# Kernel tuning notes

Measured on AMD Instinct MI355X. Metric: run time of the kernel, lower is better.

## Reference

```python
import jax, jax.numpy as jnp
import numpy as np

L, C = 32768, 512
EPS = 1e-5

def _layernorm(x, w, b):
    mu = jnp.mean(x, axis=-1, keepdims=True)
    var = jnp.mean(jnp.square(x - mu), axis=-1, keepdims=True)
    return (x - mu) * jax.lax.rsqrt(var + EPS) * w + b

def _scan(u, decay):
    # inclusive first-order linear scan: b_t = decay * b_{t-1} + u_t
    a = jnp.broadcast_to(decay, u.shape)
    def combine(l, r):
        return (l[0] * r[0], r[1] + r[0] * l[1])
    _, b = jax.lax.associative_scan(combine, (a, u), axis=0)
    return b

def setup_inputs() -> dict:
    key = jax.random.key(0)
    ks = jax.random.split(key, 8)
    s = 0.02
    return {
        "x": jax.random.normal(ks[0], (L, C), dtype=jnp.float32),
        "ln1_w": jnp.ones((C,), jnp.float32),
        "ln1_b": jnp.zeros((C,), jnp.float32),
        "W_in": jax.random.normal(ks[1], (C, C), jnp.float32) * s,
        "b_in": jnp.zeros((C,), jnp.float32),
        "W_gate": jax.random.normal(ks[2], (C, C), jnp.float32) * s,
        "b_gate": jnp.zeros((C,), jnp.float32),
        "W_out": jax.random.normal(ks[3], (C, C), jnp.float32) * s,
        "b_out": jnp.zeros((C,), jnp.float32),
        "decay_logit": jnp.zeros((C,), jnp.float32),  # torch init: zeros -> sigmoid = 0.5
        "ln2_w": jnp.ones((C,), jnp.float32),
        "ln2_b": jnp.zeros((C,), jnp.float32),
        "W_ff1": jax.random.normal(ks[4], (C, 2 * C), jnp.float32) * s,
        "b_ff1": jnp.zeros((2 * C,), jnp.float32),
        "W_ff2": jax.random.normal(ks[5], (2 * C, C), jnp.float32) * s,
        "b_ff2": jnp.zeros((C,), jnp.float32),
    }

def reference(x, ln1_w, ln1_b, W_in, b_in, W_gate, b_gate, W_out, b_out,
              decay_logit, ln2_w, ln2_b, W_ff1, b_ff1, W_ff2, b_ff2):
    hidden = _layernorm(x, ln1_w, ln1_b)
    u = hidden @ W_in + b_in
    gate = jax.nn.sigmoid(hidden @ W_gate + b_gate)
    decay = jax.nn.sigmoid(decay_logit)
    fwd = _scan(u, decay) * gate
    bwd = jnp.flip(_scan(jnp.flip(u, axis=0), decay), axis=0) * gate
    state_out = 0.5 * (fwd + bwd)
    x = x + state_out @ W_out + b_out
    h = _layernorm(x, ln2_w, ln2_b)
    x = x + jax.nn.silu(h @ W_ff1 + b_ff1) @ W_ff2 + b_ff2
    return x
```

## Files before the change

kernel.cpp:

```cpp
#include <hip/hip_runtime.h>
#include <stdint.h>


#define L_SEQ 32768
#define CDIM 512
#define LN_EPS 1e-5f
#define CHUNK 64
#define NCHUNK (L_SEQ / CHUNK)

typedef __attribute__((ext_vector_type(8))) short short8;
typedef __attribute__((ext_vector_type(4))) float floatx4;

__device__ inline unsigned short f2bf(float f) {
  union { float f; unsigned int u; } v; v.f = f;
  unsigned int r = v.u + 0x7fffu + ((v.u >> 16) & 1u);
  return (unsigned short)(r >> 16);
}
__device__ inline float bf2f(unsigned short h) {
  union { float f; unsigned int u; } v; v.u = ((unsigned int)h) << 16;
  return v.f;
}
__device__ inline float sigmoidf_(float x) { return 1.0f / (1.0f + __expf(-x)); }

__device__ __forceinline__ void gll16(const void* g, void* l) {
  __builtin_amdgcn_global_load_lds(
      (__attribute__((address_space(1))) void*)g,
      (__attribute__((address_space(3))) void*)l, 16, 0, 0);
}

__global__ __launch_bounds__(256) void ln_kernel(const float* __restrict__ x,
    const float* __restrict__ w, const float* __restrict__ b,
    unsigned short* __restrict__ out) {
  int row = blockIdx.x * 4 + (threadIdx.x >> 6);
  int lane = threadIdx.x & 63;
  const float4* xr = (const float4*)(x + (size_t)row * CDIM);
  float4 v0 = xr[lane * 2];
  float4 v1 = xr[lane * 2 + 1];
  float s = v0.x + v0.y + v0.z + v0.w + v1.x + v1.y + v1.z + v1.w;
  float s2 = v0.x * v0.x + v0.y * v0.y + v0.z * v0.z + v0.w * v0.w +
             v1.x * v1.x + v1.y * v1.y + v1.z * v1.z + v1.w * v1.w;
  for (int m = 32; m > 0; m >>= 1) {
    s += __shfl_xor(s, m, 64);
    s2 += __shfl_xor(s2, m, 64);
  }
  float mean = s * (1.0f / CDIM);
  float var = s2 * (1.0f / CDIM) - mean * mean;
  float rs = rsqrtf(var + LN_EPS);
  const float4* wr = (const float4*)w;
  const float4* br = (const float4*)b;
  float4 w0 = wr[lane * 2], w1 = wr[lane * 2 + 1];
  float4 b0 = br[lane * 2], b1 = br[lane * 2 + 1];
  unsigned int p0 = (unsigned int)f2bf((v0.x - mean) * rs * w0.x + b0.x) |
                    ((unsigned int)f2bf((v0.y - mean) * rs * w0.y + b0.y) << 16);
  unsigned int p1 = (unsigned int)f2bf((v0.z - mean) * rs * w0.z + b0.z) |
                    ((unsigned int)f2bf((v0.w - mean) * rs * w0.w + b0.w) << 16);
  unsigned int p2 = (unsigned int)f2bf((v1.x - mean) * rs * w1.x + b1.x) |
                    ((unsigned int)f2bf((v1.y - mean) * rs * w1.y + b1.y) << 16);
  unsigned int p3 = (unsigned int)f2bf((v1.z - mean) * rs * w1.z + b1.z) |
                    ((unsigned int)f2bf((v1.w - mean) * rs * w1.w + b1.w) << 16);
  uint4 pk; pk.x = p0; pk.y = p1; pk.z = p2; pk.w = p3;
  *((uint4*)(out + (size_t)row * CDIM + lane * 8)) = pk;
}

__global__ __launch_bounds__(256) void prep_all(
    const float* __restrict__ W_in, const float* __restrict__ W_gate,
    const float* __restrict__ W_out, const float* __restrict__ W_ff1,
    const float* __restrict__ W_ff2, const float* __restrict__ logit,
    unsigned short* __restrict__ Wt_ig, unsigned short* __restrict__ Wt_out,
    unsigned short* __restrict__ Wt_ff1, unsigned short* __restrict__ Wt_ff2,
    float* __restrict__ decay, float* __restrict__ decayT) {
  int b = blockIdx.x;
  if (b >= 1792) {
    for (int c = threadIdx.x; c < CDIM; c += 256) {
      float d = sigmoidf_(logit[c]);
      decay[c] = d;
      float p = d;
      for (int i = 0; i < 6; i++) p *= p;
      decayT[c] = p;
    }
    return;
  }
  const float* W; unsigned short* Wt; int Kd, Nd, t;
  if (b < 256)       { W = W_in;   Wt = Wt_ig;             Kd = 512;  Nd = 512;  t = b; }
  else if (b < 512)  { W = W_gate; Wt = Wt_ig + 512 * 512; Kd = 512;  Nd = 512;  t = b - 256; }
  else if (b < 768)  { W = W_out;  Wt = Wt_out;            Kd = 512;  Nd = 512;  t = b - 512; }
  else if (b < 1280) { W = W_ff1;  Wt = Wt_ff1;            Kd = 512;  Nd = 1024; t = b - 768; }
  else               { W = W_ff2;  Wt = Wt_ff2;            Kd = 1024; Nd = 512;  t = b - 1280; }
  int ntx = Nd >> 5;
  int n0 = (t % ntx) * 32, k0 = (t / ntx) * 32;
  __shared__ float tile[32][33];
  int tx = threadIdx.x & 31, ty = threadIdx.x >> 5;
  for (int r = 0; r < 32; r += 8)
    tile[ty + r][tx] = W[(size_t)(k0 + ty + r) * Nd + n0 + tx];
  __syncthreads();
  for (int r = 0; r < 32; r += 8)
    Wt[(size_t)(n0 + ty + r) * Kd + k0 + tx] = f2bf(tile[tx][ty + r]);
}

template <int EPI>
__global__ __launch_bounds__(256, 4) void gemm_bt(
    const unsigned short* __restrict__ A, const unsigned short* __restrict__ Bt,
    const float* __restrict__ biasA, const float* __restrict__ biasB,
    const float* __restrict__ res, float* __restrict__ outF,
    unsigned short* __restrict__ outU, unsigned short* __restrict__ outG,
    int M, int N, int K) {
  __shared__ char smemRaw[34048];
  unsigned short* As = (unsigned short*)smemRaw;
  unsigned short* Bs = (unsigned short*)(smemRaw + 16384);

  int nbx = gridDim.x, nby = gridDim.y;
  int bid = blockIdx.x + blockIdx.y * nbx;
  int per = (nbx * nby) >> 3;
  int w = (bid & 7) * per + (bid >> 3);
  int ni = w % nby;
  int mi = w / nby;
  int bm = mi << 7, bn = ni << 7;

  int tid = threadIdx.x, wave = tid >> 6, lane = tid & 63;
  int wm = (wave >> 1) * 64, wn = (wave & 1) * 64;

  int srow = wave * 16 + (lane >> 2);
  int chunkSel = (lane & 3) ^ ((lane >> 3) & 3);
  int scol = chunkSel * 8;
  const unsigned short* aP0 = A + (size_t)(bm + srow) * K + scol;
  const unsigned short* aP1 = A + (size_t)(bm + 64 + srow) * K + scol;
  const unsigned short* bP0 = Bt + (size_t)(bn + srow) * K + scol;
  const unsigned short* bP1 = Bt + (size_t)(bn + 64 + srow) * K + scol;
  int wbase = wave * 512;

#define STAGE(bufOff, ktile) do {                                 \
    int _o = (ktile) * 32;                                        \
    gll16(aP0 + _o, As + (bufOff) + wbase);                       \
    gll16(aP1 + _o, As + (bufOff) + 2048 + wbase);                \
    gll16(bP0 + _o, Bs + (bufOff) + wbase);                       \
    gll16(bP1 + _o, Bs + (bufOff) + 2048 + wbase);                \
  } while (0)

  floatx4 acc[4][4];
#pragma unroll
  for (int i = 0; i < 4; i++)
#pragma unroll
    for (int j = 0; j < 4; j++) acc[i][j] = (floatx4){0.f, 0.f, 0.f, 0.f};

  int quad = lane >> 4, r16 = lane & 15;
  int cSwz = ((quad ^ (r16 >> 1)) & 3) * 8;

  int NK = K >> 5;

  STAGE(0, 0);
  asm volatile("s_waitcnt vmcnt(0)" ::: "memory");
  __syncthreads();

  for (int k = 0; k < NK; ++k) {
    int cur = (k & 1) * 4096, nxt = cur ^ 4096;
    if (k + 1 < NK) STAGE(nxt, k + 1);
    short8 af[4], bfm[4];
#pragma unroll
    for (int i = 0; i < 4; i++)
      af[i] = *(const short8*)(&As[cur + (wm + i * 16 + r16) * 32 + cSwz]);
#pragma unroll
    for (int j = 0; j < 4; j++)
      bfm[j] = *(const short8*)(&Bs[cur + (wn + j * 16 + r16) * 32 + cSwz]);
#pragma unroll
    for (int i = 0; i < 4; i++)
#pragma unroll
      for (int j = 0; j < 4; j++)
        acc[i][j] = __builtin_amdgcn_mfma_f32_16x16x32_bf16(af[i], bfm[j], acc[i][j], 0, 0, 0);
    asm volatile("s_waitcnt vmcnt(0)" ::: "memory");
    __syncthreads();
  }
#undef STAGE

  if (EPI == 1) {
#pragma unroll
    for (int j = 0; j < 4; j++) {
      int n = bn + wn + j * 16 + r16;
#pragma unroll
      for (int i = 0; i < 4; i++) {
        int mb = bm + wm + i * 16 + quad * 4;
#pragma unroll
        for (int r = 0; r < 4; r++) {
          size_t idx = (size_t)(mb + r) * N + n;
          outF[idx] = res[idx] + acc[i][j][r] + biasA[n];
        }
      }
    }
  } else {
    unsigned short* sm = (unsigned short*)smemRaw;
#pragma unroll
    for (int j = 0; j < 4; j++) {
      int n = bn + wn + j * 16 + r16;
      int ln = wn + j * 16 + r16;
#pragma unroll
      for (int i = 0; i < 4; i++) {
        int lmb = wm + i * 16 + quad * 4;
#pragma unroll
        for (int r = 0; r < 4; r++) {
          float v = acc[i][j][r];
          float t;
          if (EPI == 0) {
            t = (n < 512) ? (v + biasA[n]) : sigmoidf_(v + biasB[n - 512]);
          } else {
            float z = v + biasA[n];
            t = z * sigmoidf_(z);
          }
          sm[(lmb + r) * 132 + ln] = f2bf(t);
        }
      }
    }
    __syncthreads();
    int row = tid >> 1, half = tid & 1;
    const unsigned short* src = sm + row * 132 + half * 64;
    unsigned short* gptr;
    if (EPI == 0) {
      gptr = ((bn < 512) ? outU : (outG - 512)) + (size_t)(bm + row) * 512 + bn + half * 64;
    } else {
      gptr = outG + (size_t)(bm + row) * N + bn + half * 64;
    }
#pragma unroll
    for (int s = 0; s < 8; s++)
      *(short8*)(gptr + s * 8) = *(const short8*)(src + s * 8);
  }
}

__global__ __launch_bounds__(512) void scan_phase1(const unsigned short* __restrict__ u,
    const float* __restrict__ decay, float* __restrict__ fa, float* __restrict__ ba) {
  int c = threadIdx.x, k = blockIdx.x;
  float d = decay[c];
  const unsigned short* up = u + (size_t)k * CHUNK * CDIM + c;
  float f = 0.f, bs = 0.f, p = 1.f;
#pragma unroll 8
  for (int t = 0; t < CHUNK; t++) {
    float v = bf2f(up[(size_t)t * CDIM]);
    f = d * f + v;
    bs += p * v;
    p *= d;
  }
  fa[(size_t)k * CDIM + c] = f;
  ba[(size_t)k * CDIM + c] = bs;
}

__global__ __launch_bounds__(256) void scan_phase2(const float* __restrict__ fa,
    const float* __restrict__ ba, const float* __restrict__ decayT,
    float* __restrict__ fc, float* __restrict__ bc) {
  int c = blockIdx.x * 256 + threadIdx.x;
  float dT = decayT[c];
  float runf = 0.f, runb = 0.f;
#pragma unroll 4
  for (int k = 0; k < NCHUNK; k++) {
    int kb = NCHUNK - 1 - k;
    fc[(size_t)k * CDIM + c] = runf;
    runf = dT * runf + fa[(size_t)k * CDIM + c];
    bc[(size_t)kb * CDIM + c] = runb;
    runb = dT * runb + ba[(size_t)kb * CDIM + c];
  }
}

__global__ __launch_bounds__(512) void scan_phase3(const unsigned short* __restrict__ u,
    const unsigned short* __restrict__ gate, const float* __restrict__ decay,
    const float* __restrict__ fc, const float* __restrict__ bc,
    unsigned short* __restrict__ state) {
  int c = threadIdx.x, k = blockIdx.x;
  float d = decay[c];
  size_t base = (size_t)k * CHUNK * CDIM + c;
  float fwd[CHUNK];
  float run = fc[(size_t)k * CDIM + c];
#pragma unroll
  for (int t = 0; t < CHUNK; t++) {
    run = d * run + bf2f(u[base + (size_t)t * CDIM]);
    fwd[t] = run;
  }
  float runb = bc[(size_t)k * CDIM + c];
#pragma unroll
  for (int t = CHUNK - 1; t >= 0; t--) {
    runb = d * runb + bf2f(u[base + (size_t)t * CDIM]);
    float g = bf2f(gate[base + (size_t)t * CDIM]);
    state[base + (size_t)t * CDIM] = f2bf(0.5f * (fwd[t] + runb) * g);
  }
}

extern "C" void kernel_launch(void* const* d_in, const int* in_sizes, int n_in,
                              void* d_out, int out_size, void* d_ws, size_t ws_size,
                              hipStream_t stream) {
  const float* x = (const float*)d_in[0];
  const float* ln1_w = (const float*)d_in[1];
  const float* ln1_b = (const float*)d_in[2];
  const float* W_in = (const float*)d_in[3];
  const float* b_in = (const float*)d_in[4];
  const float* W_gate = (const float*)d_in[5];
  const float* b_gate = (const float*)d_in[6];
  const float* W_out = (const float*)d_in[7];
  const float* b_out = (const float*)d_in[8];
  const float* decay_logit = (const float*)d_in[9];
  const float* ln2_w = (const float*)d_in[10];
  const float* ln2_b = (const float*)d_in[11];
  const float* W_ff1 = (const float*)d_in[12];
  const float* b_ff1 = (const float*)d_in[13];
  const float* W_ff2 = (const float*)d_in[14];
  const float* b_ff2 = (const float*)d_in[15];

  char* ws = (char*)d_ws;
  size_t off = 0;
  auto alloc = [&](size_t bytes) -> void* {
    void* p = ws + off;
    off += (bytes + 255) & ~(size_t)255;
    return p;
  };
  unsigned short* Wt_ig  = (unsigned short*)alloc((size_t)1024 * 512 * 2);
  unsigned short* Wt_out = (unsigned short*)alloc((size_t)512 * 512 * 2);
  unsigned short* Wt_ff1 = (unsigned short*)alloc((size_t)1024 * 512 * 2);
  unsigned short* Wt_ff2 = (unsigned short*)alloc((size_t)512 * 1024 * 2);
  float* fa = (float*)alloc((size_t)NCHUNK * CDIM * 4);
  float* ba = (float*)alloc((size_t)NCHUNK * CDIM * 4);
  float* fc = (float*)alloc((size_t)NCHUNK * CDIM * 4);
  float* bc = (float*)alloc((size_t)NCHUNK * CDIM * 4);
  float* decay  = (float*)alloc(CDIM * 4);
  float* decayT = (float*)alloc(CDIM * 4);
  const size_t LC2 = (size_t)L_SEQ * CDIM * 2;
  unsigned short* R1 = (unsigned short*)alloc(LC2);
  unsigned short* R2 = (unsigned short*)alloc(LC2);
  unsigned short* R3 = (unsigned short*)alloc(LC2);
  unsigned short* hidden = R1;
  unsigned short* state  = R1;
  unsigned short* hbuf   = R1;
  unsigned short* u_buf  = R2;
  unsigned short* gate   = R3;
  unsigned short* ffb    = R2;
  float* x2 = (float*)d_out;

  prep_all<<<1793, 256, 0, stream>>>(W_in, W_gate, W_out, W_ff1, W_ff2,
      decay_logit, Wt_ig, Wt_out, Wt_ff1, Wt_ff2, decay, decayT);

  ln_kernel<<<L_SEQ / 4, 256, 0, stream>>>(x, ln1_w, ln1_b, hidden);

  gemm_bt<0><<<dim3(L_SEQ / 128, 1024 / 128), 256, 0, stream>>>(
      hidden, Wt_ig, b_in, b_gate, nullptr, nullptr, u_buf, gate, L_SEQ, 1024, 512);

  scan_phase1<<<NCHUNK, 512, 0, stream>>>(u_buf, decay, fa, ba);
  scan_phase2<<<2, 256, 0, stream>>>(fa, ba, decayT, fc, bc);
  scan_phase3<<<NCHUNK, 512, 0, stream>>>(u_buf, gate, decay, fc, bc, state);

  gemm_bt<1><<<dim3(L_SEQ / 128, 512 / 128), 256, 0, stream>>>(
      state, Wt_out, b_out, nullptr, x, x2, nullptr, nullptr, L_SEQ, 512, 512);

  ln_kernel<<<L_SEQ / 4, 256, 0, stream>>>(x2, ln2_w, ln2_b, hbuf);

  gemm_bt<2><<<dim3(L_SEQ / 128, 1024 / 128), 256, 0, stream>>>(
      hbuf, Wt_ff1, b_ff1, nullptr, nullptr, nullptr, nullptr, ffb, L_SEQ, 1024, 512);

  gemm_bt<1><<<dim3(L_SEQ / 128, 512 / 128), 256, 0, stream>>>(
      ffb, Wt_ff2, b_ff2, nullptr, x2, x2, nullptr, nullptr, L_SEQ, 512, 1024);
}
```

Baseline: 466.6 us.

## Split serial chunk-carry scan into hierarchical two-level scan and cache u in registers

The single serial phase-2 scan over 512 chunks, which ran on only 2 blocks, is replaced by a two-level scan. Sixteen groups each scan 32 chunks in parallel, then a single block scans the 16 group totals. Phase 3 folds the group carry in using decay powers computed by binary exponentiation. Phase 3 also keeps the bf16 u values packed in registers for the backward pass instead of reloading them from global memory, at the cost of extra register pressure and one more kernel launch.

```diff
diff --git a/kernel.cpp b/kernel.cpp
--- a/kernel.cpp
+++ b/kernel.cpp
@@ -7,6 +7,8 @@
 #define LN_EPS 1e-5f
 #define CHUNK 64
 #define NCHUNK (L_SEQ / CHUNK)
+#define NGRP 16
+#define GCHUNK (NCHUNK / NGRP)
 
 typedef __attribute__((ext_vector_type(8))) short short8;
 typedef __attribute__((ext_vector_type(4))) float floatx4;
@@ -21,6 +23,13 @@
   return v.f;
 }
 __device__ inline float sigmoidf_(float x) { return 1.0f / (1.0f + __expf(-x)); }
+
+__device__ inline float powi5(float s, int e) {
+  float p = 1.f;
+#pragma unroll
+  for (int b = 0; b < 5; b++) { if (e & (1 << b)) p *= s; s *= s; }
+  return p;
+}
 
 __device__ __forceinline__ void gll16(const void* g, void* l) {
   __builtin_amdgcn_global_load_lds(
@@ -240,42 +249,84 @@
   ba[(size_t)k * CDIM + c] = bs;
 }
 
-__global__ __launch_bounds__(256) void scan_phase2(const float* __restrict__ fa,
+__global__ __launch_bounds__(512) void scan_p2a(const float* __restrict__ fa,
     const float* __restrict__ ba, const float* __restrict__ decayT,
-    float* __restrict__ fc, float* __restrict__ bc) {
-  int c = blockIdx.x * 256 + threadIdx.x;
+    float* __restrict__ fc, float* __restrict__ bc,
+    float* __restrict__ gaF, float* __restrict__ gaB) {
+  int c = threadIdx.x, g = blockIdx.x;
   float dT = decayT[c];
-  float runf = 0.f, runb = 0.f;
+  int k0 = g * GCHUNK;
+  float runf = 0.f;
 #pragma unroll 4
-  for (int k = 0; k < NCHUNK; k++) {
-    int kb = NCHUNK - 1 - k;
-    fc[(size_t)k * CDIM + c] = runf;
-    runf = dT * runf + fa[(size_t)k * CDIM + c];
-    bc[(size_t)kb * CDIM + c] = runb;
-    runb = dT * runb + ba[(size_t)kb * CDIM + c];
+  for (int j = 0; j < GCHUNK; j++) {
+    size_t idx = (size_t)(k0 + j) * CDIM + c;
+    fc[idx] = runf;
+    runf = dT * runf + fa[idx];
+  }
+  gaF[(size_t)g * CDIM + c] = runf;
+  float runb = 0.f;
+#pragma unroll 4
+  for (int j = GCHUNK - 1; j >= 0; j--) {
+    size_t idx = (size_t)(k0 + j) * CDIM + c;
+    bc[idx] = runb;
+    runb = dT * runb + ba[idx];
+  }
+  gaB[(size_t)g * CDIM + c] = runb;
+}
+
+__global__ __launch_bounds__(512) void scan_p2b(const float* __restrict__ gaF,
+    const float* __restrict__ gaB, const float* __restrict__ decayT,
+    float* __restrict__ GF, float* __restrict__ GB) {
+  int c = threadIdx.x;
+  float dT = decayT[c];
+  float d32 = dT;
+#pragma unroll
+  for (int i = 0; i < 5; i++) d32 *= d32;
+  float gf = 0.f;
+#pragma unroll
+  for (int g = 0; g < NGRP; g++) {
+    GF[(size_t)g * CDIM + c] = gf;
+    gf = d32 * gf + gaF[(size_t)g * CDIM + c];
+  }
+  float gb = 0.f;
+#pragma unroll
+  for (int g = NGRP - 1; g >= 0; g--) {
+    GB[(size_t)g * CDIM + c] = gb;
+    gb = d32 * gb + gaB[(size_t)g * CDIM + c];
   }
 }
 
 __global__ __launch_bounds__(512) void scan_phase3(const unsigned short* __restrict__ u,
     const unsigned short* __restrict__ gate, const float* __restrict__ decay,
-    const float* __restrict__ fc, const float* __restrict__ bc,
-    unsigned short* __restrict__ state) {
+    const float* __restrict__ decayT, const float* __restrict__ fc,
+    const float* __restrict__ bc, const float* __restrict__ GF,
+    const float* __restrict__ GB, unsigned short* __restrict__ state) {
   int c = threadIdx.x, k = blockIdx.x;
+  int g = k >> 5, j = k & 31;
   float d = decay[c];
+  float dT = decayT[c];
   size_t base = (size_t)k * CHUNK * CDIM + c;
+  size_t kc = (size_t)k * CDIM + c;
+  size_t gc = (size_t)g * CDIM + c;
+  float run  = fc[kc] + powi5(dT, j) * GF[gc];
+  float runb0 = bc[kc] + powi5(dT, 31 - j) * GB[gc];
   float fwd[CHUNK];
-  float run = fc[(size_t)k * CDIM + c];
+  unsigned int us[CHUNK / 2];
 #pragma unroll
   for (int t = 0; t < CHUNK; t++) {
-    run = d * run + bf2f(u[base + (size_t)t * CDIM]);
+    unsigned short uv = u[base + (size_t)t * CDIM];
+    if (t & 1) us[t >> 1] |= ((unsigned int)uv) << 16;
+    else       us[t >> 1] = uv;
+    run = d * run + bf2f(uv);
     fwd[t] = run;
   }
-  float runb = bc[(size_t)k * CDIM + c];
+  float runb = runb0;
 #pragma unroll
   for (int t = CHUNK - 1; t >= 0; t--) {
-    runb = d * runb + bf2f(u[base + (size_t)t * CDIM]);
-    float g = bf2f(gate[base + (size_t)t * CDIM]);
-    state[base + (size_t)t * CDIM] = f2bf(0.5f * (fwd[t] + runb) * g);
+    unsigned short uv = (unsigned short)((us[t >> 1] >> ((t & 1) * 16)) & 0xffffu);
+    runb = d * runb + bf2f(uv);
+    float gv = bf2f(gate[base + (size_t)t * CDIM]);
+    state[base + (size_t)t * CDIM] = f2bf(0.5f * (fwd[t] + runb) * gv);
   }
 }
 
@@ -314,6 +365,10 @@
   float* ba = (float*)alloc((size_t)NCHUNK * CDIM * 4);
   float* fc = (float*)alloc((size_t)NCHUNK * CDIM * 4);
   float* bc = (float*)alloc((size_t)NCHUNK * CDIM * 4);
+  float* gaF = (float*)alloc((size_t)NGRP * CDIM * 4);
+  float* gaB = (float*)alloc((size_t)NGRP * CDIM * 4);
+  float* GFb = (float*)alloc((size_t)NGRP * CDIM * 4);
+  float* GBb = (float*)alloc((size_t)NGRP * CDIM * 4);
   float* decay  = (float*)alloc(CDIM * 4);
   float* decayT = (float*)alloc(CDIM * 4);
   const size_t LC2 = (size_t)L_SEQ * CDIM * 2;
@@ -337,8 +392,10 @@
       hidden, Wt_ig, b_in, b_gate, nullptr, nullptr, u_buf, gate, L_SEQ, 1024, 512);
 
   scan_phase1<<<NCHUNK, 512, 0, stream>>>(u_buf, decay, fa, ba);
-  scan_phase2<<<2, 256, 0, stream>>>(fa, ba, decayT, fc, bc);
-  scan_phase3<<<NCHUNK, 512, 0, stream>>>(u_buf, gate, decay, fc, bc, state);
+  scan_p2a<<<NGRP, 512, 0, stream>>>(fa, ba, decayT, fc, bc, gaF, gaB);
+  scan_p2b<<<1, 512, 0, stream>>>(gaF, gaB, decayT, GFb, GBb);
+  scan_phase3<<<NCHUNK, 512, 0, stream>>>(u_buf, gate, decay, decayT, fc, bc,
+      GFb, GBb, state);
 
   gemm_bt<1><<<dim3(L_SEQ / 128, 512 / 128), 256, 0, stream>>>(
       state, Wt_out, b_out, nullptr, x, x2, nullptr, nullptr, L_SEQ, 512, 512);
```

After: 431.4 us. -7.5%, faster.
